# Kernel tuning notes

Measured on AMD Instinct MI355X. Metric: run time of the kernel, lower is better.

Reference implementation:

```python
import jax, jax.numpy as jnp
import numpy as np

DIM = 512
NUM_HEADS = 8
HEAD_DIM = DIM // NUM_HEADS


def setup_inputs() -> dict:
    key = jax.random.key(0)
    ks = jax.random.split(key, 9)
    s = 1.0 / np.sqrt(DIM)
    x = jax.random.normal(ks[0], (2, 4096, DIM), dtype=jnp.float32)
    Wq = jax.random.uniform(ks[1], (DIM, DIM), jnp.float32, -s, s)
    bq = jax.random.uniform(ks[2], (DIM,), jnp.float32, -s, s)
    Wk = jax.random.uniform(ks[3], (DIM, DIM), jnp.float32, -s, s)
    bk = jax.random.uniform(ks[4], (DIM,), jnp.float32, -s, s)
    Wv = jax.random.uniform(ks[5], (DIM, DIM), jnp.float32, -s, s)
    bv = jax.random.uniform(ks[6], (DIM,), jnp.float32, -s, s)
    Wo = jax.random.uniform(ks[7], (DIM, DIM), jnp.float32, -s, s)
    bo = jax.random.uniform(ks[8], (DIM,), jnp.float32, -s, s)
    return {"x": x, "Wq": Wq, "bq": bq, "Wk": Wk, "bk": bk,
            "Wv": Wv, "bv": bv, "Wo": Wo, "bo": bo}


def reference(x, Wq, bq, Wk, bk, Wv, bv, Wo, bo):
    B, S, D = x.shape
    H, Hd = NUM_HEADS, HEAD_DIM
    # Linear layers (torch stores weight as [out,in]; here W is [in,out])
    q = (x @ Wq + bq).reshape(B, S, H, Hd).transpose(0, 2, 1, 3)  # [B,H,S,Hd]
    k = (x @ Wk + bk).reshape(B, S, H, Hd).transpose(0, 2, 1, 3)
    v = (x @ Wv + bv).reshape(B, S, H, Hd).transpose(0, 2, 1, 3)
    # NOTE: original scales by dim**0.5, not head_dim**0.5
    energy = jnp.einsum('bhqd,bhkd->bhqk', q, k) / jnp.sqrt(jnp.float32(D))
    attn = jax.nn.softmax(energy, axis=-1)
    out = jnp.einsum('bhqk,bhkd->bhqd', attn, v)
    out = out.transpose(0, 2, 1, 3).reshape(B, S, D)
    return out @ Wo + bo
```

## Files before the change

### kernel.cpp

```cpp
#include <hip/hip_runtime.h>

typedef unsigned short USH;
typedef short s16x8 __attribute__((ext_vector_type(8)));
typedef float f32x4 __attribute__((ext_vector_type(4)));
typedef float f32x4v __attribute__((ext_vector_type(4)));
typedef unsigned int u32x4 __attribute__((ext_vector_type(4)));
typedef s16x8 s16x8_a __attribute__((may_alias));
typedef f32x4v f32x4v_a __attribute__((may_alias));
typedef u32x4 u32x4_a __attribute__((may_alias));
typedef unsigned long long u64_a __attribute__((may_alias));

#if __has_builtin(__builtin_amdgcn_exp2f)
#define EXP2F(x) __builtin_amdgcn_exp2f(x)
#else
#define EXP2F(x) __builtin_exp2f(x)
#endif

__device__ __forceinline__ USH f2bf(float f) {
  union { float f; unsigned int i; } c; c.f = f;
  unsigned int x = c.i;
  return (USH)((x + 0x7FFFu + ((x >> 16) & 1u)) >> 16);
}
__device__ __forceinline__ unsigned int pk_bf16(float a, float b) {
#if __has_builtin(__builtin_amdgcn_cvt_pk_bf16_f32)
  typedef USH ush2 __attribute__((ext_vector_type(2)));
  union { ush2 v; unsigned int u; } r;
  r.v = __builtin_amdgcn_cvt_pk_bf16_f32(a, b);
  return r.u;
#else
  union { float f; unsigned int i; } ca, cb; ca.f = a; cb.f = b;
  return ((ca.i + 0x8000u) >> 16) | ((cb.i + 0x8000u) & 0xFFFF0000u);
#endif
}

__device__ __forceinline__ f32x4 mfma16(s16x8 a, s16x8 b, f32x4 c) {
  return __builtin_amdgcn_mfma_f32_16x16x32_bf16(a, b, c, 0, 0, 0);
}

#if __has_builtin(__builtin_amdgcn_global_load_lds)
__device__ __forceinline__ void gld_lds16(const USH* g, USH* l) {
  __builtin_amdgcn_global_load_lds(
      static_cast<const unsigned int __attribute__((address_space(1)))*>(
          (const void __attribute__((address_space(1)))*)g),
      static_cast<unsigned int __attribute__((address_space(3)))*>(
          (void __attribute__((address_space(3)))*)l),
      16, 0, 0);
}
#else
__device__ __forceinline__ void gld_lds16(const USH* g, USH* l) {
  *(s16x8_a*)l = *(const s16x8_a*)g;
}
#endif

__global__ __launch_bounds__(256) void prep(
    const float* __restrict__ Wq, const float* __restrict__ Wk,
    const float* __restrict__ Wv, const float* __restrict__ Wo,
    const float* __restrict__ x, USH* __restrict__ wsT, USH* __restrict__ xb) {
  __shared__ float tile[32][33];
  const int z = blockIdx.z;
  const int t = threadIdx.x;
  if (z == 4) {
    const size_t b0 = ((size_t)blockIdx.y * 16 + blockIdx.x) * 16384;
    #pragma unroll
    for (int j = 0; j < 8; ++j) {
      const size_t i = b0 + (size_t)j * 2048 + t * 8;
      const f32x4v a = *(const f32x4v_a*)(x + i);
      const f32x4v b = *(const f32x4v_a*)(x + i + 4);
      u32x4 s;
      s.x = pk_bf16(a.x, a.y); s.y = pk_bf16(a.z, a.w);
      s.z = pk_bf16(b.x, b.y); s.w = pk_bf16(b.z, b.w);
      *(u32x4_a*)(xb + i) = s;
    }
    return;
  }
  const float* W = (z == 0) ? Wq : (z == 1) ? Wk : (z == 2) ? Wv : Wo;
  USH* WT = wsT + (size_t)z * 262144;
  const int n0 = blockIdx.x * 32, k0 = blockIdx.y * 32;
  const int tx = t & 31, ty = t >> 5;
  #pragma unroll
  for (int i = 0; i < 4; ++i)
    tile[ty + i * 8][tx] = W[(size_t)(k0 + ty + i * 8) * 512 + n0 + tx];
  __syncthreads();
  #pragma unroll
  for (int i = 0; i < 4; ++i)
    WT[(size_t)(n0 + ty + i * 8) * 512 + k0 + tx] = f2bf(tile[tx][ty + i * 8]);
}

template <int MODE>
__global__ __launch_bounds__(256, 3) void gemm_bias(
    const USH* __restrict__ A, const USH* __restrict__ BT0,
    const float* __restrict__ b0, const float* __restrict__ b1,
    const float* __restrict__ b2,
    USH* __restrict__ oQ, USH* __restrict__ oKV, float* __restrict__ oF) {
  __shared__ __align__(16) USH As[8192];
  __shared__ __align__(16) USH Bs[8192];
  const int z = blockIdx.z;
  const USH* BT = BT0 + (size_t)z * 262144;
  const float* bias = (z == 0) ? b0 : ((z == 1) ? b1 : b2);
  USH* outb = (z == 0) ? oQ : (oKV + (size_t)(z - 1) * 4194304);
  const float qs = (MODE == 1 && z == 0) ? 0.06375871528132839f : 1.0f;

  const int t = threadIdx.x;
  const int w = t >> 6, lane = t & 63;
  const int c = lane & 15, g = lane >> 4;
  const int wm = w & 1, wn = w >> 1;
  const int m0 = blockIdx.x * 128, n0 = blockIdx.y * 128;

  f32x4 acc[4][4] = {};

  const int rD = w * 32 + (lane >> 3);
  const int ccD = (((lane & 7) ^ ((lane >> 3) & 7))) * 8;
  const USH* ApD = A + (size_t)(m0 + rD) * 512 + ccD;
  const USH* BpD = BT + (size_t)(n0 + rD) * 512 + ccD;
  USH* lA = As + w * 2048 + lane * 8;
  USH* lB = Bs + w * 2048 + lane * 8;

  for (int kt = 0; kt < 8; ++kt) {
    __syncthreads();
    #pragma unroll
    for (int j = 0; j < 4; ++j) {
      gld_lds16(ApD + kt * 64 + j * 4096, lA + j * 512);
      gld_lds16(BpD + kt * 64 + j * 4096, lB + j * 512);
    }
    __syncthreads();
    #pragma unroll
    for (int ks = 0; ks < 2; ++ks) {
      s16x8 af[4], bfr[4];
      #pragma unroll
      for (int i = 0; i < 4; ++i) {
        const int ra = wm * 64 + i * 16 + c;
        const int rb = wn * 64 + i * 16 + c;
        af[i]  = *(const s16x8_a*)(As + ra * 64 + ((ks * 4 + g) ^ (ra & 7)) * 8);
        bfr[i] = *(const s16x8_a*)(Bs + rb * 64 + ((ks * 4 + g) ^ (rb & 7)) * 8);
      }
      #pragma unroll
      for (int mf = 0; mf < 4; ++mf)
        #pragma unroll
        for (int nf = 0; nf < 4; ++nf)
          acc[mf][nf] = mfma16(af[mf], bfr[nf], acc[mf][nf]);
    }
  }

  #pragma unroll
  for (int nf = 0; nf < 4; ++nf) {
    const int n = n0 + wn * 64 + nf * 16 + c;
    const float bv = bias[n];
    #pragma unroll
    for (int mf = 0; mf < 4; ++mf)
      #pragma unroll
      for (int r = 0; r < 4; ++r) {
        const int m = m0 + wm * 64 + mf * 16 + g * 4 + r;
        const float v = (acc[mf][nf][r] + bv) * qs;
        if (MODE == 0) {
          oF[(size_t)m * 512 + n] = v;
        } else {
          const int bb = m >> 12, s = m & 4095, h = n >> 6, hd = n & 63;
          if (z == 2)
            outb[(((size_t)(bb * 8 + h)) * 64 + hd) * 4096 + s] = f2bf(v);
          else
            outb[(((size_t)(bb * 8 + h)) * 4096 + s) * 64 + hd] = f2bf(v);
        }
      }
  }
}

__global__ __launch_bounds__(512, 2) void attn(const USH* __restrict__ Qbuf,
                                               const USH* __restrict__ kv,
                                               USH* __restrict__ att) {
  __shared__ __align__(16) USH Ks[2 * 8192];
  __shared__ __align__(16) USH Vt[2 * 8192];
  __shared__ __align__(16) USH Ps[8][32 * 140];
  __shared__ float lbuf[8][32];

  const int t = threadIdx.x;
  const int w = t >> 6, lane = t & 63;
  const int c = lane & 15, g = lane >> 4;
  const int linear = blockIdx.x + (blockIdx.y << 4);
  const int xcd = linear & 7, idx = linear >> 3;
  const int bh = xcd + ((idx >> 4) << 3);
  const int bb = bh >> 3, hh = bh & 7;
  const size_t base = (size_t)bh * 262144;
  const USH* Q = Qbuf + base;
  const USH* K = kv + base;
  const USH* V = kv + 4194304 + base;
  const int q0 = (idx & 15) * 256 + w * 32;

  s16x8 qf[2][2];
  #pragma unroll
  for (int qi = 0; qi < 2; ++qi)
    #pragma unroll
    for (int kh = 0; kh < 2; ++kh)
      qf[qi][kh] = *(const s16x8_a*)(Q + (size_t)(q0 + qi * 16 + c) * 64 + kh * 32 + g * 8);

  s16x8 onesf;
  {
    const short one = (short)0x3F80, val = (c == 0) ? one : (short)0;
    #pragma unroll
    for (int j = 0; j < 8; ++j) onesf[j] = val;
  }

  f32x4 o[2][4] = {};
  f32x4 o_l[2] = {};

  const int keyK = w * 16 + (lane >> 2);
  const int ccK = (lane & 3) ^ ((keyK >> 1) & 3);
  const USH* gK0 = K + (size_t)keyK * 64 + ccK * 8;
  const int hdV = w * 4 + (lane >> 4);
  const int ccV = (lane & 15) ^ (hdV & 7);
  const USH* gV0 = V + (size_t)hdV * 4096 + ccV * 8;
  USH* lK = Ks + w * 512 + lane * 8;
  USH* lV = Vt + w * 512 + lane * 8;

  #pragma unroll
  for (int j = 0; j < 2; ++j) {
    gld_lds16(gK0 + j * 32, lK + j * 4096);
    gld_lds16(gV0 + (size_t)j * 131072, lV + j * 4096);
  }

  for (int kt = 0; kt < 32; ++kt) {
    const int buf = kt & 1;
    __syncthreads();
    if (kt < 31) {
      const int nb = (buf ^ 1) * 8192;
      #pragma unroll
      for (int j = 0; j < 2; ++j) {
        gld_lds16(gK0 + (size_t)(kt + 1) * 8192 + j * 32, lK + nb + j * 4096);
        gld_lds16(gV0 + (size_t)(kt + 1) * 128 + (size_t)j * 131072, lV + nb + j * 4096);
      }
    }

    f32x4 st[2][8] = {};
    #pragma unroll
    for (int kh = 0; kh < 2; ++kh) {
      s16x8 ak[8];
      #pragma unroll
      for (int kff = 0; kff < 8; ++kff) {
        const int row = kff * 16 + c;
        const int qsw = (g ^ ((c >> 1) & 3)) * 8;
        ak[kff] = *(const s16x8_a*)(Ks + buf * 8192 + kh * 4096 + row * 32 + qsw);
      }
      #pragma unroll
      for (int qi = 0; qi < 2; ++qi)
        #pragma unroll
        for (int kff = 0; kff < 8; ++kff)
          st[qi][kff] = mfma16(ak[kff], qf[qi][kh], st[qi][kff]);
    }

    #pragma unroll
    for (int qi = 0; qi < 2; ++qi)
      #pragma unroll
      for (int kff = 0; kff < 8; ++kff) {
        #pragma unroll
        for (int r = 0; r < 4; ++r) st[qi][kff][r] = EXP2F(st[qi][kff][r]);
        const unsigned int lo = pk_bf16(st[qi][kff][0], st[qi][kff][1]);
        const unsigned int hi = pk_bf16(st[qi][kff][2], st[qi][kff][3]);
        *(u64_a*)(&Ps[w][(qi * 16 + c) * 140 + kff * 16 + g * 4]) =
            (unsigned long long)lo | ((unsigned long long)hi << 32);
      }

    #pragma unroll
    for (int kf = 0; kf < 4; ++kf) {
      s16x8 ap[2];
      #pragma unroll
      for (int qi = 0; qi < 2; ++qi)
        ap[qi] = *(const s16x8_a*)(&Ps[w][(qi * 16 + c) * 140 + kf * 32 + g * 8]);
      s16x8 bv[4];
      #pragma unroll
      for (int hf = 0; hf < 4; ++hf) {
        const int qv = (((kf * 4 + g) ^ (c & 7))) * 8;
        bv[hf] = *(const s16x8_a*)(Vt + buf * 8192 + (c + 16 * hf) * 128 + qv);
      }
      #pragma unroll
      for (int qi = 0; qi < 2; ++qi) {
        #pragma unroll
        for (int hf = 0; hf < 4; ++hf)
          o[qi][hf] = mfma16(ap[qi], bv[hf], o[qi][hf]);
        o_l[qi] = mfma16(ap[qi], onesf, o_l[qi]);
      }
    }
  }

  if (c == 0) {
    #pragma unroll
    for (int qi = 0; qi < 2; ++qi)
      #pragma unroll
      for (int r = 0; r < 4; ++r) lbuf[w][qi * 16 + g * 4 + r] = o_l[qi][r];
  }
  __syncthreads();

  #pragma unroll
  for (int qi = 0; qi < 2; ++qi)
    #pragma unroll
    for (int r = 0; r < 4; ++r) {
      const int ml = qi * 16 + g * 4 + r;
      const float linv = 1.0f / lbuf[w][ml];
      const int qrow = q0 + ml;
      #pragma unroll
      for (int hf = 0; hf < 4; ++hf) {
        const int hd = c + 16 * hf;
        att[((size_t)(bb * 4096 + qrow)) * 512 + hh * 64 + hd] =
            f2bf(o[qi][hf][r] * linv);
      }
    }
}

extern "C" void kernel_launch(void* const* d_in, const int* in_sizes, int n_in,
                              void* d_out, int out_size, void* d_ws, size_t ws_size,
                              hipStream_t stream) {
  (void)in_sizes; (void)n_in; (void)out_size; (void)ws_size;
  const float* x  = (const float*)d_in[0];
  const float* Wq = (const float*)d_in[1];
  const float* bq = (const float*)d_in[2];
  const float* Wk = (const float*)d_in[3];
  const float* bk = (const float*)d_in[4];
  const float* Wv = (const float*)d_in[5];
  const float* bv = (const float*)d_in[6];
  const float* Wo = (const float*)d_in[7];
  const float* bo = (const float*)d_in[8];
  USH* ws  = (USH*)d_ws;
  USH* wT  = ws;
  USH* kv  = ws + 1048576;
  USH* att = ws + 1048576 + 8388608;
  float* outF = (float*)d_out;
  USH* qscratch = (USH*)d_out;
  USH* xb = (USH*)d_out + 4194304;

  prep<<<dim3(16, 16, 5), 256, 0, stream>>>(Wq, Wk, Wv, Wo, x, wT, xb);
  gemm_bias<1><<<dim3(64, 4, 3), 256, 0, stream>>>(xb, wT, bq, bk, bv,
                                                   qscratch, kv, nullptr);
  attn<<<dim3(16, 16), 512, 0, stream>>>(qscratch, kv, att);
  gemm_bias<0><<<dim3(64, 4, 1), 256, 0, stream>>>(att, wT + 3 * 262144, bo, bo, bo,
                                                   nullptr, nullptr, outF);
}
```

Measured before the change: 199.9 us.

## Fuse fp32-to-bf16 conversion of x into QKV GEMM A-tile loads

Removes the separate x conversion pass from the prep kernel and has the QKV projection GEMM load fp32 x tiles directly into LDS with an XOR swizzle, converting to bf16 when fragments are read. This drops one full write and read of a bf16 copy of x. In exchange, the QKV GEMM reads twice as many bytes for A (reread by each of the 4 column blocks and 3 z-slices), uses double the LDS for the A tile, which may lower occupancy, and adds conversion ALU work in the inner loop.

```diff
diff --git a/kernel.cpp b/kernel.cpp
--- a/kernel.cpp
+++ b/kernel.cpp
@@ -38,7 +38,7 @@
 }
 
 #if __has_builtin(__builtin_amdgcn_global_load_lds)
-__device__ __forceinline__ void gld_lds16(const USH* g, USH* l) {
+__device__ __forceinline__ void gld_lds16(const void* g, void* l) {
   __builtin_amdgcn_global_load_lds(
       static_cast<const unsigned int __attribute__((address_space(1)))*>(
           (const void __attribute__((address_space(1)))*)g),
@@ -47,7 +47,7 @@
       16, 0, 0);
 }
 #else
-__device__ __forceinline__ void gld_lds16(const USH* g, USH* l) {
+__device__ __forceinline__ void gld_lds16(const void* g, void* l) {
   *(s16x8_a*)l = *(const s16x8_a*)g;
 }
 #endif
@@ -55,24 +55,10 @@
 __global__ __launch_bounds__(256) void prep(
     const float* __restrict__ Wq, const float* __restrict__ Wk,
     const float* __restrict__ Wv, const float* __restrict__ Wo,
-    const float* __restrict__ x, USH* __restrict__ wsT, USH* __restrict__ xb) {
+    USH* __restrict__ wsT) {
   __shared__ float tile[32][33];
   const int z = blockIdx.z;
   const int t = threadIdx.x;
-  if (z == 4) {
-    const size_t b0 = ((size_t)blockIdx.y * 16 + blockIdx.x) * 16384;
-    #pragma unroll
-    for (int j = 0; j < 8; ++j) {
-      const size_t i = b0 + (size_t)j * 2048 + t * 8;
-      const f32x4v a = *(const f32x4v_a*)(x + i);
-      const f32x4v b = *(const f32x4v_a*)(x + i + 4);
-      u32x4 s;
-      s.x = pk_bf16(a.x, a.y); s.y = pk_bf16(a.z, a.w);
-      s.z = pk_bf16(b.x, b.y); s.w = pk_bf16(b.z, b.w);
-      *(u32x4_a*)(xb + i) = s;
-    }
-    return;
-  }
   const float* W = (z == 0) ? Wq : (z == 1) ? Wk : (z == 2) ? Wv : Wo;
   USH* WT = wsT + (size_t)z * 262144;
   const int n0 = blockIdx.x * 32, k0 = blockIdx.y * 32;
@@ -88,11 +74,12 @@
 
 template <int MODE>
 __global__ __launch_bounds__(256, 3) void gemm_bias(
-    const USH* __restrict__ A, const USH* __restrict__ BT0,
+    const USH* __restrict__ A, const float* __restrict__ A32,
+    const USH* __restrict__ BT0,
     const float* __restrict__ b0, const float* __restrict__ b1,
     const float* __restrict__ b2,
     USH* __restrict__ oQ, USH* __restrict__ oKV, float* __restrict__ oF) {
-  __shared__ __align__(16) USH As[8192];
+  __shared__ __align__(16) USH As[MODE == 1 ? 16384 : 8192];
   __shared__ __align__(16) USH Bs[8192];
   const int z = blockIdx.z;
   const USH* BT = BT0 + (size_t)z * 262144;
@@ -108,19 +95,40 @@
 
   f32x4 acc[4][4] = {};
 
-  const int rD = w * 32 + (lane >> 3);
-  const int ccD = (((lane & 7) ^ ((lane >> 3) & 7))) * 8;
-  const USH* ApD = A + (size_t)(m0 + rD) * 512 + ccD;
-  const USH* BpD = BT + (size_t)(n0 + rD) * 512 + ccD;
-  USH* lA = As + w * 2048 + lane * 8;
+  const int rB = w * 32 + (lane >> 3);
+  const int ccB = (((lane & 7) ^ ((lane >> 3) & 7))) * 8;
+  const USH* BpD = BT + (size_t)(n0 + rB) * 512 + ccB;
   USH* lB = Bs + w * 2048 + lane * 8;
+
+  const USH* ApD = nullptr;
+  USH* lA0 = nullptr;
+  const float* Ap32 = nullptr;
+  USH* lA1 = nullptr;
+  if (MODE == 0) {
+    ApD = A + (size_t)(m0 + rB) * 512 + ccB;
+    lA0 = As + w * 2048 + lane * 8;
+  } else {
+    const int rA = w * 4 + (lane >> 4);
+    const int gcA = (lane & 15) ^ (rA & 15);
+    Ap32 = A32 + (size_t)(m0 + rA) * 512 + gcA * 4;
+    lA1 = As + w * 512 + lane * 8;
+  }
 
   for (int kt = 0; kt < 8; ++kt) {
     __syncthreads();
-    #pragma unroll
-    for (int j = 0; j < 4; ++j) {
-      gld_lds16(ApD + kt * 64 + j * 4096, lA + j * 512);
-      gld_lds16(BpD + kt * 64 + j * 4096, lB + j * 512);
+    if (MODE == 0) {
+      #pragma unroll
+      for (int j = 0; j < 4; ++j) {
+        gld_lds16(ApD + kt * 64 + j * 4096, lA0 + j * 512);
+        gld_lds16(BpD + kt * 64 + j * 4096, lB + j * 512);
+      }
+    } else {
+      #pragma unroll
+      for (int j = 0; j < 8; ++j)
+        gld_lds16(Ap32 + kt * 64 + (size_t)j * 8192, lA1 + j * 2048);
+      #pragma unroll
+      for (int j = 0; j < 4; ++j)
+        gld_lds16(BpD + kt * 64 + j * 4096, lB + j * 512);
     }
     __syncthreads();
     #pragma unroll
@@ -130,7 +138,19 @@
       for (int i = 0; i < 4; ++i) {
         const int ra = wm * 64 + i * 16 + c;
         const int rb = wn * 64 + i * 16 + c;
-        af[i]  = *(const s16x8_a*)(As + ra * 64 + ((ks * 4 + g) ^ (ra & 7)) * 8);
+        if (MODE == 0) {
+          af[i] = *(const s16x8_a*)(As + ra * 64 + ((ks * 4 + g) ^ (ra & 7)) * 8);
+        } else {
+          const int e = ks * 4 + g;
+          const int p0 = (2 * e) ^ (ra & 15), p1 = (2 * e + 1) ^ (ra & 15);
+          const float* Af = (const float*)As + ra * 64;
+          const f32x4v lo = *(const f32x4v_a*)(Af + p0 * 4);
+          const f32x4v hi = *(const f32x4v_a*)(Af + p1 * 4);
+          union { u32x4 u; s16x8 v; } cvt;
+          cvt.u.x = pk_bf16(lo.x, lo.y); cvt.u.y = pk_bf16(lo.z, lo.w);
+          cvt.u.z = pk_bf16(hi.x, hi.y); cvt.u.w = pk_bf16(hi.z, hi.w);
+          af[i] = cvt.v;
+        }
         bfr[i] = *(const s16x8_a*)(Bs + rb * 64 + ((ks * 4 + g) ^ (rb & 7)) * 8);
       }
       #pragma unroll
@@ -323,12 +343,12 @@
   USH* att = ws + 1048576 + 8388608;
   float* outF = (float*)d_out;
   USH* qscratch = (USH*)d_out;
-  USH* xb = (USH*)d_out + 4194304;
-
-  prep<<<dim3(16, 16, 5), 256, 0, stream>>>(Wq, Wk, Wv, Wo, x, wT, xb);
-  gemm_bias<1><<<dim3(64, 4, 3), 256, 0, stream>>>(xb, wT, bq, bk, bv,
+
+  prep<<<dim3(16, 16, 4), 256, 0, stream>>>(Wq, Wk, Wv, Wo, wT);
+  gemm_bias<1><<<dim3(64, 4, 3), 256, 0, stream>>>(nullptr, x, wT, bq, bk, bv,
                                                    qscratch, kv, nullptr);
   attn<<<dim3(16, 16), 512, 0, stream>>>(qscratch, kv, att);
-  gemm_bias<0><<<dim3(64, 4, 1), 256, 0, stream>>>(att, wT + 3 * 262144, bo, bo, bo,
+  gemm_bias<0><<<dim3(64, 4, 1), 256, 0, stream>>>(att, nullptr, wT + 3 * 262144,
+                                                   bo, bo, bo,
                                                    nullptr, nullptr, outF);
 }
```

Result: slower. 204.0 us (median of 2 runs) (+2.1%).
